# Kernel optimization log

Hardware: AMD Instinct MI355X
Metric: run time of the kernel (lower is better)

Reference implementation:

```python
import jax, jax.numpy as jnp
import numpy as np

N = 2048      # number of ROIs
C = 1024      # in_channels == inter_channels
G = 16        # groups
D = C // G    # per-group dim = 64


def _bbox_overlaps(b1, b2):
    # mmdet-1.x IoU with +1 pixel convention; b1:(N,4), b2:(M,4)
    area1 = (b1[:, 2] - b1[:, 0] + 1) * (b1[:, 3] - b1[:, 1] + 1)  # (N,)
    area2 = (b2[:, 2] - b2[:, 0] + 1) * (b2[:, 3] - b2[:, 1] + 1)  # (M,)
    lt = jnp.maximum(b1[:, None, :2], b2[None, :, :2])             # (N,M,2)
    rb = jnp.minimum(b1[:, None, 2:], b2[None, :, 2:])             # (N,M,2)
    wh = jnp.clip(rb - lt + 1, 0)
    inter = wh[..., 0] * wh[..., 1]                                # (N,M)
    return inter / (area1[:, None] + area2[None, :] - inter)


def setup_inputs() -> dict:
    key = jax.random.key(0)
    ks = jax.random.split(key, 9)
    in_x = jax.random.normal(ks[0], (N, C), dtype=jnp.float32)
    # valid boxes: [batch_idx, x1, y1, x2, y2]
    xy = jax.random.uniform(ks[1], (N, 2), minval=0.0, maxval=800.0)
    wh = jax.random.uniform(ks[2], (N, 2), minval=8.0, maxval=200.0)
    rois = jnp.concatenate([jnp.zeros((N, 1)), xy, xy + wh], axis=1).astype(jnp.float32)
    s = 1.0 / np.sqrt(C)
    W0 = jax.random.normal(ks[3], (C, C), dtype=jnp.float32) * s
    b0 = jnp.zeros((C,), dtype=jnp.float32)
    W1 = jax.random.normal(ks[4], (C, C), dtype=jnp.float32) * s
    b1 = jnp.zeros((C,), dtype=jnp.float32)
    # grouped 1x1 conv: per group maps C channels -> D channels
    Wout = jax.random.normal(ks[5], (G, D, C), dtype=jnp.float32) * s
    bout = jnp.zeros((C,), dtype=jnp.float32)
    return {"in_x": in_x, "rois": rois, "W0": W0, "b0": b0, "W1": W1,
            "b1": b1, "Wout": Wout, "bout": bout}


def reference(in_x, rois, W0, b0, W1, b1, Wout, bout):
    # self-attention path: in_ref_x = in_x, ref_rois = rois
    # embed convs are pre-activation (relu -> 1x1 conv), shared for x and ref_x
    def embed(v):
        v = jax.nn.relu(v) @ W0.T + b0
        v = jax.nn.relu(v) @ W1.T + b1
        return v
    x = embed(in_x)                      # (N, C)
    ref_x = x                            # shared convs, same input
    xg = x.reshape(N, G, D)
    rg = ref_x.reshape(N, G, D)
    scores = jnp.einsum('ngd,mgd->ngm', xg, rg) / jnp.sqrt(jnp.float32(D))  # (N,G,N)
    ious = _bbox_overlaps(rois[:, 1:], rois[:, 1:])                          # (N,N)
    scores = scores + jnp.log(ious[:, None, :] + 1e-6)
    attn = jax.nn.softmax(scores, axis=2)                                    # (N,G,N)
    y = jnp.einsum('ngm,mc->ngc', attn, in_x)                                # (N,G,C)
    out = jnp.einsum('ngc,goc->ngo', y, Wout).reshape(N, C) + bout           # (N,C)
    return out
```

## Files before the change

### kernel.cpp

```cpp
#include <hip/hip_runtime.h>
#include <math.h>

constexpr int NROI = 2048;
constexpr int CDIM = 1024;
constexpr int NG   = 16;
constexpr int DH   = 64;

typedef __attribute__((ext_vector_type(8))) short short8;
typedef __attribute__((ext_vector_type(4))) float floatx4;

#define MFMA_BF16(a, b, c) __builtin_amdgcn_mfma_f32_16x16x32_bf16((a), (b), (c), 0, 0, 0)

__device__ __forceinline__ short f2bf(float f) {
  unsigned u = __float_as_uint(f);
  unsigned r = 0x7fffu + ((u >> 16) & 1u);
  return (short)((u + r) >> 16);
}
__device__ __forceinline__ float bf2f(unsigned short u) {
  return __uint_as_float(((unsigned)u) << 16);
}
__device__ __forceinline__ unsigned pack2(float a, float b) {
  return (unsigned)(unsigned short)f2bf(a) | ((unsigned)(unsigned short)f2bf(b) << 16);
}

typedef __attribute__((address_space(1))) void GV;
typedef __attribute__((address_space(3))) void LV;
__device__ __forceinline__ void gl2lds16(const void* g, void* l) {
  __builtin_amdgcn_global_load_lds((GV*)g, (LV*)l, 16, 0, 0);
}

__device__ __forceinline__ short8 brelu(short8 v) {
  union { short8 s; unsigned u[4]; } x; x.s = v;
#pragma unroll
  for (int i = 0; i < 4; ++i) {
    unsigned m = (x.u[i] >> 15) & 0x10001u;
    x.u[i] &= ~(m * 0xFFFFu);
  }
  return x.s;
}

__global__ __launch_bounds__(256) void convert_kernel(
    const float* __restrict__ in_x, const float* __restrict__ W0,
    const float* __restrict__ W1, const float* __restrict__ Wout,
    short* __restrict__ xin_b, short* __restrict__ W0b,
    short* __restrict__ W1b, short* __restrict__ Woutb)
{
  const int i = blockIdx.x * 256 + threadIdx.x;
  {
    const float4 v = ((const float4*)in_x)[i];
    uint2 u; u.x = pack2(v.x, v.y); u.y = pack2(v.z, v.w);
    ((uint2*)xin_b)[i] = u;
  }
  if (i < 262144) {
    float4 v = ((const float4*)W0)[i];
    uint2 u; u.x = pack2(v.x, v.y); u.y = pack2(v.z, v.w);
    ((uint2*)W0b)[i] = u;
    v = ((const float4*)W1)[i];
    u.x = pack2(v.x, v.y); u.y = pack2(v.z, v.w);
    ((uint2*)W1b)[i] = u;
    v = ((const float4*)Wout)[i];
    u.x = pack2(v.x, v.y); u.y = pack2(v.z, v.w);
    ((uint2*)Woutb)[i] = u;
  }
}

__global__ __launch_bounds__(256) void iou_kernel(const float* __restrict__ rois,
                                                  unsigned short* __restrict__ biasb)
{
  const int q = blockIdx.y;
  const int k = blockIdx.x * 256 + threadIdx.x;
  const float qx1 = rois[q * 5 + 1], qy1 = rois[q * 5 + 2];
  const float qx2 = rois[q * 5 + 3], qy2 = rois[q * 5 + 4];
  const float qa = (qx2 - qx1 + 1.f) * (qy2 - qy1 + 1.f);
  const float kx1 = rois[k * 5 + 1], ky1 = rois[k * 5 + 2];
  const float kx2 = rois[k * 5 + 3], ky2 = rois[k * 5 + 4];
  const float ka = (kx2 - kx1 + 1.f) * (ky2 - ky1 + 1.f);
  float iw = fminf(qx2, kx2) - fmaxf(qx1, kx1) + 1.f;
  float ih = fminf(qy2, ky2) - fmaxf(qy1, ky1) + 1.f;
  iw = fmaxf(iw, 0.f); ih = fmaxf(ih, 0.f);
  const float inter = iw * ih;
  const float iou = inter / (qa + ka - inter);
  biasb[(size_t)q * NROI + k] = (unsigned short)f2bf(iou + 1e-6f);
}

__global__ __launch_bounds__(256) void gemm_bf16(
    const short* __restrict__ A, const short* __restrict__ B,
    const float* __restrict__ bias, short* __restrict__ C,
    int M, int Nn, int K, int reluA, int transOut)
{
  __shared__ short As[8 * 512];
  __shared__ short Bs[8 * 512];
  const int t = threadIdx.x, w = t >> 6, lane = t & 63;
  const int wm = w >> 1, wn = w & 1;
  const int row0 = blockIdx.y * 64, col0 = blockIdx.x * 64;
  const int rlo = lane & 15, khi = (lane >> 4) * 8;

  floatx4 acc[2][2];
#pragma unroll
  for (int i = 0; i < 2; ++i)
#pragma unroll
    for (int j = 0; j < 2; ++j) acc[i][j] = (floatx4){0.f, 0.f, 0.f, 0.f};

  for (int k0 = 0; k0 < K; k0 += 64) {
    __syncthreads();
#pragma unroll
    for (int kh = 0; kh < 2; ++kh) {
      gl2lds16(A + (size_t)(row0 + w * 16 + rlo) * K + k0 + kh * 32 + khi,
               &As[(w * 2 + kh) * 512]);
      gl2lds16(B + (size_t)(col0 + w * 16 + rlo) * K + k0 + kh * 32 + khi,
               &Bs[(w * 2 + kh) * 512]);
    }
    __syncthreads();
#pragma unroll
    for (int kh = 0; kh < 2; ++kh) {
      short8 a0 = *(const short8*)&As[((wm * 2 + 0) * 2 + kh) * 512 + lane * 8];
      short8 a1 = *(const short8*)&As[((wm * 2 + 1) * 2 + kh) * 512 + lane * 8];
      if (reluA) { a0 = brelu(a0); a1 = brelu(a1); }
      const short8 b0 = *(const short8*)&Bs[((wn * 2 + 0) * 2 + kh) * 512 + lane * 8];
      const short8 b1 = *(const short8*)&Bs[((wn * 2 + 1) * 2 + kh) * 512 + lane * 8];
      acc[0][0] = MFMA_BF16(a0, b0, acc[0][0]);
      acc[0][1] = MFMA_BF16(a0, b1, acc[0][1]);
      acc[1][0] = MFMA_BF16(a1, b0, acc[1][0]);
      acc[1][1] = MFMA_BF16(a1, b1, acc[1][1]);
    }
  }

  const int colL = lane & 15, qq = lane >> 4;
  float bj[2] = {0.f, 0.f};
  if (bias) {
    bj[0] = bias[col0 + wn * 32 + colL];
    bj[1] = bias[col0 + wn * 32 + 16 + colL];
  }
#pragma unroll
  for (int i = 0; i < 2; ++i)
#pragma unroll
    for (int j = 0; j < 2; ++j)
#pragma unroll
      for (int r = 0; r < 4; ++r) {
        const int row = row0 + wm * 32 + i * 16 + qq * 4 + r;
        const int cc  = col0 + wn * 32 + j * 16 + colL;
        const short bv = f2bf(acc[i][j][r] + bj[j]);
        if (transOut) C[(size_t)cc * M + row] = bv;
        else          C[(size_t)row * Nn + cc] = bv;
      }
}

__global__ __launch_bounds__(512) void attn_bias(
    const short* __restrict__ Xb,
    const short* __restrict__ ZTb,
    const unsigned short* __restrict__ biasb,
    const float* __restrict__ bout,
    float* __restrict__ Out)
{
  const int g  = blockIdx.y;
  const int n0 = blockIdx.x * 128;
  const int t  = threadIdx.x;
  const int w    = t >> 6;
  const int lane = t & 63;
  const int col  = lane & 15;
  const int qq   = lane >> 4;
  const int t16 = (w >> 1) * 16;
  const int h32 = (w & 1) * 32;
  const int rlo = lane & 15, khi = (lane >> 4) * 8;

  __shared__ short Kf[2][8 * 512];
  __shared__ short Vf[2][8 * 512];
  __shared__ short Pf[8 * 1024];

  const size_t qoff = (size_t)(n0 + w * 16 + col) * CDIM + g * DH;
  const short8 qf0 = *(const short8*)(Xb + qoff + qq * 8);
  const short8 qf1 = *(const short8*)(Xb + qoff + 32 + qq * 8);

  floatx4 oc[4];
#pragma unroll
  for (int dt = 0; dt < 4; ++dt) oc[dt] = (floatx4){0.f, 0.f, 0.f, 0.f};
  float lsum[4] = {0.f, 0.f, 0.f, 0.f};

  gl2lds16(Xb + (size_t)(t16 + rlo) * CDIM + g * DH + h32 + khi, &Kf[0][w * 512]);
  gl2lds16(ZTb + (size_t)(g * DH + t16 + rlo) * NROI + h32 + khi, &Vf[0][w * 512]);
  __syncthreads();

  for (int it = 0; it < NROI / 64; ++it) {
    const int p  = it & 1;
    const int m0 = it * 64;
    if (it + 1 < NROI / 64) {
      const int m1 = m0 + 64;
      gl2lds16(Xb + (size_t)(m1 + t16 + rlo) * CDIM + g * DH + h32 + khi,
               &Kf[1 - p][w * 512]);
      gl2lds16(ZTb + (size_t)(g * DH + t16 + rlo) * NROI + m1 + h32 + khi,
               &Vf[1 - p][w * 512]);
    }

    float bb[4][4];
#pragma unroll
    for (int ct = 0; ct < 4; ++ct)
#pragma unroll
      for (int r = 0; r < 4; ++r)
        bb[ct][r] = bf2f(biasb[(size_t)(n0 + w * 16 + qq * 4 + r) * NROI +
                               m0 + ct * 16 + col]);

    floatx4 sc[4];
#pragma unroll
    for (int ct = 0; ct < 4; ++ct) {
      const short8 b0 = *(const short8*)&Kf[p][(ct * 2 + 0) * 512 + lane * 8];
      const short8 b1 = *(const short8*)&Kf[p][(ct * 2 + 1) * 512 + lane * 8];
      floatx4 z4 = (floatx4){0.f, 0.f, 0.f, 0.f};
      z4 = MFMA_BF16(qf0, b0, z4);
      z4 = MFMA_BF16(qf1, b1, z4);
      sc[ct] = z4;
    }

#pragma unroll
    for (int ct = 0; ct < 4; ++ct)
#pragma unroll
      for (int r = 0; r < 4; ++r)
        sc[ct][r] = __expf(sc[ct][r] * 0.125f) * bb[ct][r];
#pragma unroll
    for (int r = 0; r < 4; ++r)
      lsum[r] += sc[0][r] + sc[1][r] + sc[2][r] + sc[3][r];

    {
      short* pw = &Pf[w * 1024];
#pragma unroll
      for (int ct = 0; ct < 4; ++ct) {
        const int key = ct * 16 + col;
        const int base = (key >> 5) * 512 + (key & 7);
#pragma unroll
        for (int r = 0; r < 4; ++r) {
          const int dl = (4 * qq + r) + ((key >> 3) & 3) * 16;
          pw[base + dl * 8] = f2bf(sc[ct][r]);
        }
      }
      const short8 pa0 = *(const short8*)&pw[0 * 512 + lane * 8];
      const short8 pa1 = *(const short8*)&pw[1 * 512 + lane * 8];
#pragma unroll
      for (int dt = 0; dt < 4; ++dt) {
        const short8 v0 = *(const short8*)&Vf[p][(dt * 2 + 0) * 512 + lane * 8];
        const short8 v1 = *(const short8*)&Vf[p][(dt * 2 + 1) * 512 + lane * 8];
        oc[dt] = MFMA_BF16(pa0, v0, oc[dt]);
        oc[dt] = MFMA_BF16(pa1, v1, oc[dt]);
      }
    }
    __syncthreads();
  }

#pragma unroll
  for (int r = 0; r < 4; ++r) {
    float s = lsum[r];
    s += __shfl_xor(s, 1); s += __shfl_xor(s, 2);
    s += __shfl_xor(s, 4); s += __shfl_xor(s, 8);
    lsum[r] = s;
  }
#pragma unroll
  for (int dt = 0; dt < 4; ++dt) {
    const float bo = bout[g * DH + dt * 16 + col];
#pragma unroll
    for (int r = 0; r < 4; ++r)
      Out[(size_t)(n0 + w * 16 + qq * 4 + r) * CDIM + g * DH + dt * 16 + col] =
          oc[dt][r] / lsum[r] + bo;
  }
}

__global__ __launch_bounds__(256) void attn_inline(
    const short* __restrict__ Xb, const short* __restrict__ ZTb,
    const float* __restrict__ rois, const float* __restrict__ bout,
    float* __restrict__ Out)
{
  const int g = blockIdx.y, n0 = blockIdx.x * 64;
  const int t = threadIdx.x, w = t >> 6, lane = t & 63;
  const int col = lane & 15, qq = lane >> 4;

  __shared__ short Kf[8 * 512];
  __shared__ short Vf[8 * 512];
  __shared__ short Pf[4 * 1024];
  __shared__ float Bsb[64 * 5];

  const size_t qoff = (size_t)(n0 + w * 16 + col) * CDIM + g * DH;
  const short8 qf0 = *(const short8*)(Xb + qoff + qq * 8);
  const short8 qf1 = *(const short8*)(Xb + qoff + 32 + qq * 8);

  float qx1[4], qy1[4], qx2[4], qy2[4], qar[4];
#pragma unroll
  for (int r = 0; r < 4; ++r) {
    const float* rb = rois + (size_t)(n0 + w * 16 + qq * 4 + r) * 5;
    qx1[r] = rb[1]; qy1[r] = rb[2]; qx2[r] = rb[3]; qy2[r] = rb[4];
    qar[r] = (qx2[r] - qx1[r] + 1.f) * (qy2[r] - qy1[r] + 1.f);
  }

  floatx4 oc[4];
#pragma unroll
  for (int dt = 0; dt < 4; ++dt) oc[dt] = (floatx4){0.f, 0.f, 0.f, 0.f};
  float lsum[4] = {0.f, 0.f, 0.f, 0.f};

  for (int m0 = 0; m0 < NROI; m0 += 64) {
    __syncthreads();
#pragma unroll
    for (int ss = 0; ss < 2; ++ss) {
      const int s = t + ss * 256;
      {
        const int key = s >> 3, d0 = (s & 7) * 8;
        const int fr = (key >> 4) * 2 + (d0 >> 5);
        const int dl = (key & 15) + ((d0 >> 3) & 3) * 16;
        *(short8*)&Kf[fr * 512 + dl * 8] =
            *(const short8*)(Xb + (size_t)(m0 + key) * CDIM + g * DH + d0);
      }
      {
        const int d = s >> 3, k0 = (s & 7) * 8;
        const int fr = (d >> 4) * 2 + (k0 >> 5);
        const int dl = (d & 15) + ((k0 >> 3) & 3) * 16;
        *(short8*)&Vf[fr * 512 + dl * 8] =
            *(const short8*)(ZTb + (size_t)(g * DH + d) * NROI + m0 + k0);
      }
    }
    if (t < 64) {
      const float* rb = rois + (size_t)(m0 + t) * 5;
      const float x1 = rb[1], y1 = rb[2], x2 = rb[3], y2 = rb[4];
      Bsb[t * 5 + 0] = x1; Bsb[t * 5 + 1] = y1;
      Bsb[t * 5 + 2] = x2; Bsb[t * 5 + 3] = y2;
      Bsb[t * 5 + 4] = (x2 - x1 + 1.f) * (y2 - y1 + 1.f);
    }
    __syncthreads();

    floatx4 sc[4];
#pragma unroll
    for (int ct = 0; ct < 4; ++ct) {
      const short8 b0 = *(const short8*)&Kf[(ct * 2 + 0) * 512 + lane * 8];
      const short8 b1 = *(const short8*)&Kf[(ct * 2 + 1) * 512 + lane * 8];
      floatx4 z4 = (floatx4){0.f, 0.f, 0.f, 0.f};
      z4 = MFMA_BF16(qf0, b0, z4);
      z4 = MFMA_BF16(qf1, b1, z4);
      sc[ct] = z4;
    }
#pragma unroll
    for (int ct = 0; ct < 4; ++ct) {
      const int k = ct * 16 + col;
      const float kx1 = Bsb[k * 5 + 0], ky1 = Bsb[k * 5 + 1];
      const float kx2 = Bsb[k * 5 + 2], ky2 = Bsb[k * 5 + 3], ka = Bsb[k * 5 + 4];
#pragma unroll
      for (int r = 0; r < 4; ++r) {
        float iw = fminf(qx2[r], kx2) - fmaxf(qx1[r], kx1) + 1.f;
        float ih = fminf(qy2[r], ky2) - fmaxf(qy1[r], ky1) + 1.f;
        iw = fmaxf(iw, 0.f); ih = fmaxf(ih, 0.f);
        const float inter = iw * ih;
        const float iou = inter * __builtin_amdgcn_rcpf(qar[r] + ka - inter);
        sc[ct][r] = __expf(sc[ct][r] * 0.125f) * (iou + 1e-6f);
      }
    }
#pragma unroll
    for (int r = 0; r < 4; ++r)
      lsum[r] += sc[0][r] + sc[1][r] + sc[2][r] + sc[3][r];
    {
      short* pw = &Pf[w * 1024];
#pragma unroll
      for (int ct = 0; ct < 4; ++ct) {
        const int key = ct * 16 + col;
        const int base = (key >> 5) * 512 + (key & 7);
#pragma unroll
        for (int r = 0; r < 4; ++r) {
          const int dl = (4 * qq + r) + ((key >> 3) & 3) * 16;
          pw[base + dl * 8] = f2bf(sc[ct][r]);
        }
      }
      const short8 pa0 = *(const short8*)&pw[0 * 512 + lane * 8];
      const short8 pa1 = *(const short8*)&pw[1 * 512 + lane * 8];
#pragma unroll
      for (int dt = 0; dt < 4; ++dt) {
        const short8 v0 = *(const short8*)&Vf[(dt * 2 + 0) * 512 + lane * 8];
        const short8 v1 = *(const short8*)&Vf[(dt * 2 + 1) * 512 + lane * 8];
        oc[dt] = MFMA_BF16(pa0, v0, oc[dt]);
        oc[dt] = MFMA_BF16(pa1, v1, oc[dt]);
      }
    }
  }

#pragma unroll
  for (int r = 0; r < 4; ++r) {
    float s = lsum[r];
    s += __shfl_xor(s, 1); s += __shfl_xor(s, 2);
    s += __shfl_xor(s, 4); s += __shfl_xor(s, 8);
    lsum[r] = s;
  }
#pragma unroll
  for (int dt = 0; dt < 4; ++dt) {
    const float bo = bout[g * DH + dt * 16 + col];
#pragma unroll
    for (int r = 0; r < 4; ++r)
      Out[(size_t)(n0 + w * 16 + qq * 4 + r) * CDIM + g * DH + dt * 16 + col] =
          oc[dt][r] / lsum[r] + bo;
  }
}

extern "C" void kernel_launch(void* const* d_in, const int* in_sizes, int n_in,
                              void* d_out, int out_size, void* d_ws, size_t ws_size,
                              hipStream_t stream) {
  const float* in_x = (const float*)d_in[0];
  const float* rois = (const float*)d_in[1];
  const float* W0   = (const float*)d_in[2];
  const float* b0   = (const float*)d_in[3];
  const float* W1   = (const float*)d_in[4];
  const float* b1   = (const float*)d_in[5];
  const float* Wout = (const float*)d_in[6];
  const float* bout = (const float*)d_in[7];
  float* out = (float*)d_out;
  char* w8 = (char*)d_ws;

  short* xin_b = (short*)(w8);
  short* W0b   = (short*)(w8 + (4u << 20));
  short* W1b   = (short*)(w8 + (6u << 20));
  short* Woutb = (short*)(w8 + (8u << 20));
  short* zT    = (short*)(w8 + (10u << 20));
  unsigned short* biasb = (unsigned short*)(w8 + (14u << 20));
  short* xb  = xin_b;
  short* t0b = (short*)d_out;
  const bool useBias = ws_size >= ((size_t)22u << 20);

  convert_kernel<<<2048, 256, 0, stream>>>(in_x, W0, W1, Wout,
                                           xin_b, W0b, W1b, Woutb);
  if (useBias)
    iou_kernel<<<dim3(NROI / 256, NROI), 256, 0, stream>>>(rois, biasb);

  const dim3 gg(CDIM / 64, NROI / 64);
  gemm_bf16<<<gg, 256, 0, stream>>>(xin_b, W0b, b0, t0b,
                                    NROI, CDIM, CDIM, 1, 0);
  gemm_bf16<<<gg, 256, 0, stream>>>(xin_b, Woutb, nullptr, zT,
                                    NROI, CDIM, CDIM, 0, 1);
  gemm_bf16<<<gg, 256, 0, stream>>>(t0b, W1b, b1, xb,
                                    NROI, CDIM, CDIM, 1, 0);

  if (useBias)
    attn_bias<<<dim3(NROI / 128, NG), 512, 0, stream>>>(xb, zT, biasb, bout, out);
  else
    attn_inline<<<dim3(NROI / 64, NG), 256, 0, stream>>>(xb, zT, rois, bout, out);
}
```

Baseline: 200.2 us.

## Split attention over key halves, fuse first GEMMs, transpose IoU bias loads

The attention kernel is split along the key dimension into two halves, doubling the number of blocks. Each half writes partial outputs (fp32 for one, bf16 for the other) and row sums, and a new merge kernel normalises them and adds the output bias. The IoU bias is read through the matrix's symmetry as contiguous uint2 vectors, prefetched one tile ahead. The two GEMMs that share the input are fused into one launch, and workspace buffers are reused in place. The costs are an extra merge pass, bf16 rounding of one partial sum, a larger fixed workspace requirement, and removal of the inline-IoU fallback path.

```diff
diff --git a/kernel.cpp b/kernel.cpp
--- a/kernel.cpp
+++ b/kernel.cpp
@@ -15,9 +15,6 @@
   unsigned u = __float_as_uint(f);
   unsigned r = 0x7fffu + ((u >> 16) & 1u);
   return (short)((u + r) >> 16);
-}
-__device__ __forceinline__ float bf2f(unsigned short u) {
-  return __uint_as_float(((unsigned)u) << 16);
 }
 __device__ __forceinline__ unsigned pack2(float a, float b) {
   return (unsigned)(unsigned short)f2bf(a) | ((unsigned)(unsigned short)f2bf(b) << 16);
@@ -83,10 +80,74 @@
   biasb[(size_t)q * NROI + k] = (unsigned short)f2bf(iou + 1e-6f);
 }
 
-__global__ __launch_bounds__(256) void gemm_bf16(
+__global__ __launch_bounds__(256) void gemm_fusedA(
+    const short* __restrict__ A, const short* __restrict__ BW0,
+    const short* __restrict__ BWout, const float* __restrict__ b0,
+    short* __restrict__ t0b, short* __restrict__ zT)
+{
+  __shared__ short As[8 * 512];
+  __shared__ short Bs[8 * 512];
+  const int isW0 = blockIdx.x < 16;
+  const int col0 = (blockIdx.x & 15) * 64;
+  const short* B = isW0 ? BW0 : BWout;
+  const int t = threadIdx.x, w = t >> 6, lane = t & 63;
+  const int wm = w >> 1, wn = w & 1;
+  const int row0 = blockIdx.y * 64;
+  const int rlo = lane & 15, khi = (lane >> 4) * 8;
+
+  floatx4 acc[2][2];
+#pragma unroll
+  for (int i = 0; i < 2; ++i)
+#pragma unroll
+    for (int j = 0; j < 2; ++j) acc[i][j] = (floatx4){0.f, 0.f, 0.f, 0.f};
+
+  for (int k0 = 0; k0 < CDIM; k0 += 64) {
+    __syncthreads();
+#pragma unroll
+    for (int kh = 0; kh < 2; ++kh) {
+      gl2lds16(A + (size_t)(row0 + w * 16 + rlo) * CDIM + k0 + kh * 32 + khi,
+               &As[(w * 2 + kh) * 512]);
+      gl2lds16(B + (size_t)(col0 + w * 16 + rlo) * CDIM + k0 + kh * 32 + khi,
+               &Bs[(w * 2 + kh) * 512]);
+    }
+    __syncthreads();
+#pragma unroll
+    for (int kh = 0; kh < 2; ++kh) {
+      short8 a0 = *(const short8*)&As[((wm * 2 + 0) * 2 + kh) * 512 + lane * 8];
+      short8 a1 = *(const short8*)&As[((wm * 2 + 1) * 2 + kh) * 512 + lane * 8];
+      if (isW0) { a0 = brelu(a0); a1 = brelu(a1); }
+      const short8 b0f = *(const short8*)&Bs[((wn * 2 + 0) * 2 + kh) * 512 + lane * 8];
+      const short8 b1f = *(const short8*)&Bs[((wn * 2 + 1) * 2 + kh) * 512 + lane * 8];
+      acc[0][0] = MFMA_BF16(a0, b0f, acc[0][0]);
+      acc[0][1] = MFMA_BF16(a0, b1f, acc[0][1]);
+      acc[1][0] = MFMA_BF16(a1, b0f, acc[1][0]);
+      acc[1][1] = MFMA_BF16(a1, b1f, acc[1][1]);
+    }
+  }
+
+  const int colL = lane & 15, qq = lane >> 4;
+  float bj[2] = {0.f, 0.f};
+  if (isW0) {
+    bj[0] = b0[col0 + wn * 32 + colL];
+    bj[1] = b0[col0 + wn * 32 + 16 + colL];
+  }
+#pragma unroll
+  for (int i = 0; i < 2; ++i)
+#pragma unroll
+    for (int j = 0; j < 2; ++j)
+#pragma unroll
+      for (int r = 0; r < 4; ++r) {
+        const int row = row0 + wm * 32 + i * 16 + qq * 4 + r;
+        const int cc  = col0 + wn * 32 + j * 16 + colL;
+        const short bv = f2bf(acc[i][j][r] + bj[j]);
+        if (isW0) t0b[(size_t)row * CDIM + cc] = bv;
+        else      zT[(size_t)cc * NROI + row] = bv;
+      }
+}
+
+__global__ __launch_bounds__(256) void gemm_relu_nt(
     const short* __restrict__ A, const short* __restrict__ B,
-    const float* __restrict__ bias, short* __restrict__ C,
-    int M, int Nn, int K, int reluA, int transOut)
+    const float* __restrict__ bias, short* __restrict__ C)
 {
   __shared__ short As[8 * 512];
   __shared__ short Bs[8 * 512];
@@ -101,13 +162,13 @@
 #pragma unroll
     for (int j = 0; j < 2; ++j) acc[i][j] = (floatx4){0.f, 0.f, 0.f, 0.f};
 
-  for (int k0 = 0; k0 < K; k0 += 64) {
+  for (int k0 = 0; k0 < CDIM; k0 += 64) {
     __syncthreads();
 #pragma unroll
     for (int kh = 0; kh < 2; ++kh) {
-      gl2lds16(A + (size_t)(row0 + w * 16 + rlo) * K + k0 + kh * 32 + khi,
+      gl2lds16(A + (size_t)(row0 + w * 16 + rlo) * CDIM + k0 + kh * 32 + khi,
                &As[(w * 2 + kh) * 512]);
-      gl2lds16(B + (size_t)(col0 + w * 16 + rlo) * K + k0 + kh * 32 + khi,
+      gl2lds16(B + (size_t)(col0 + w * 16 + rlo) * CDIM + k0 + kh * 32 + khi,
                &Bs[(w * 2 + kh) * 512]);
     }
     __syncthreads();
@@ -115,22 +176,20 @@
     for (int kh = 0; kh < 2; ++kh) {
       short8 a0 = *(const short8*)&As[((wm * 2 + 0) * 2 + kh) * 512 + lane * 8];
       short8 a1 = *(const short8*)&As[((wm * 2 + 1) * 2 + kh) * 512 + lane * 8];
-      if (reluA) { a0 = brelu(a0); a1 = brelu(a1); }
-      const short8 b0 = *(const short8*)&Bs[((wn * 2 + 0) * 2 + kh) * 512 + lane * 8];
-      const short8 b1 = *(const short8*)&Bs[((wn * 2 + 1) * 2 + kh) * 512 + lane * 8];
-      acc[0][0] = MFMA_BF16(a0, b0, acc[0][0]);
-      acc[0][1] = MFMA_BF16(a0, b1, acc[0][1]);
-      acc[1][0] = MFMA_BF16(a1, b0, acc[1][0]);
-      acc[1][1] = MFMA_BF16(a1, b1, acc[1][1]);
+      a0 = brelu(a0); a1 = brelu(a1);
+      const short8 b0f = *(const short8*)&Bs[((wn * 2 + 0) * 2 + kh) * 512 + lane * 8];
+      const short8 b1f = *(const short8*)&Bs[((wn * 2 + 1) * 2 + kh) * 512 + lane * 8];
+      acc[0][0] = MFMA_BF16(a0, b0f, acc[0][0]);
+      acc[0][1] = MFMA_BF16(a0, b1f, acc[0][1]);
+      acc[1][0] = MFMA_BF16(a1, b0f, acc[1][0]);
+      acc[1][1] = MFMA_BF16(a1, b1f, acc[1][1]);
     }
   }
 
   const int colL = lane & 15, qq = lane >> 4;
-  float bj[2] = {0.f, 0.f};
-  if (bias) {
-    bj[0] = bias[col0 + wn * 32 + colL];
-    bj[1] = bias[col0 + wn * 32 + 16 + colL];
-  }
+  float bj[2];
+  bj[0] = bias[col0 + wn * 32 + colL];
+  bj[1] = bias[col0 + wn * 32 + 16 + colL];
 #pragma unroll
   for (int i = 0; i < 2; ++i)
 #pragma unroll
@@ -139,28 +198,24 @@
       for (int r = 0; r < 4; ++r) {
         const int row = row0 + wm * 32 + i * 16 + qq * 4 + r;
         const int cc  = col0 + wn * 32 + j * 16 + colL;
-        const short bv = f2bf(acc[i][j][r] + bj[j]);
-        if (transOut) C[(size_t)cc * M + row] = bv;
-        else          C[(size_t)row * Nn + cc] = bv;
+        C[(size_t)row * CDIM + cc] = f2bf(acc[i][j][r] + bj[j]);
       }
 }
 
-__global__ __launch_bounds__(512) void attn_bias(
+__global__ __launch_bounds__(512) void attn_split(
     const short* __restrict__ Xb,
     const short* __restrict__ ZTb,
     const unsigned short* __restrict__ biasb,
-    const float* __restrict__ bout,
-    float* __restrict__ Out)
+    float* __restrict__ O0, short* __restrict__ O1,
+    float* __restrict__ lsums)
 {
   const int g  = blockIdx.y;
   const int n0 = blockIdx.x * 128;
-  const int t  = threadIdx.x;
-  const int w    = t >> 6;
-  const int lane = t & 63;
-  const int col  = lane & 15;
-  const int qq   = lane >> 4;
-  const int t16 = (w >> 1) * 16;
-  const int h32 = (w & 1) * 32;
+  const int sp = blockIdx.z;
+  const int mbase = sp * 1024;
+  const int t = threadIdx.x, w = t >> 6, lane = t & 63;
+  const int col = lane & 15, qq = lane >> 4;
+  const int t16 = (w >> 1) * 16, h32 = (w & 1) * 32;
   const int rlo = lane & 15, khi = (lane >> 4) * 8;
 
   __shared__ short Kf[2][8 * 512];
@@ -176,28 +231,29 @@
   for (int dt = 0; dt < 4; ++dt) oc[dt] = (floatx4){0.f, 0.f, 0.f, 0.f};
   float lsum[4] = {0.f, 0.f, 0.f, 0.f};
 
-  gl2lds16(Xb + (size_t)(t16 + rlo) * CDIM + g * DH + h32 + khi, &Kf[0][w * 512]);
-  gl2lds16(ZTb + (size_t)(g * DH + t16 + rlo) * NROI + h32 + khi, &Vf[0][w * 512]);
+  const int qrow0 = n0 + w * 16 + qq * 4;
+
+  uint2 bbc[4], bbn[4];
+#pragma unroll
+  for (int ct = 0; ct < 4; ++ct)
+    bbc[ct] = *(const uint2*)(biasb + (size_t)(mbase + ct * 16 + col) * NROI + qrow0);
+
+  gl2lds16(Xb + (size_t)(mbase + t16 + rlo) * CDIM + g * DH + h32 + khi, &Kf[0][w * 512]);
+  gl2lds16(ZTb + (size_t)(g * DH + t16 + rlo) * NROI + mbase + h32 + khi, &Vf[0][w * 512]);
   __syncthreads();
 
-  for (int it = 0; it < NROI / 64; ++it) {
-    const int p  = it & 1;
-    const int m0 = it * 64;
-    if (it + 1 < NROI / 64) {
-      const int m1 = m0 + 64;
+  for (int it = 0; it < 16; ++it) {
+    const int p = it & 1;
+    if (it < 15) {
+      const int m1 = mbase + (it + 1) * 64;
       gl2lds16(Xb + (size_t)(m1 + t16 + rlo) * CDIM + g * DH + h32 + khi,
                &Kf[1 - p][w * 512]);
       gl2lds16(ZTb + (size_t)(g * DH + t16 + rlo) * NROI + m1 + h32 + khi,
                &Vf[1 - p][w * 512]);
-    }
-
-    float bb[4][4];
-#pragma unroll
-    for (int ct = 0; ct < 4; ++ct)
-#pragma unroll
-      for (int r = 0; r < 4; ++r)
-        bb[ct][r] = bf2f(biasb[(size_t)(n0 + w * 16 + qq * 4 + r) * NROI +
-                               m0 + ct * 16 + col]);
+#pragma unroll
+      for (int ct = 0; ct < 4; ++ct)
+        bbn[ct] = *(const uint2*)(biasb + (size_t)(m1 + ct * 16 + col) * NROI + qrow0);
+    }
 
     floatx4 sc[4];
 #pragma unroll
@@ -211,10 +267,13 @@
     }
 
 #pragma unroll
-    for (int ct = 0; ct < 4; ++ct)
-#pragma unroll
-      for (int r = 0; r < 4; ++r)
-        sc[ct][r] = __expf(sc[ct][r] * 0.125f) * bb[ct][r];
+    for (int ct = 0; ct < 4; ++ct) {
+      const unsigned ux = bbc[ct].x, uy = bbc[ct].y;
+      sc[ct][0] = __expf(sc[ct][0] * 0.125f) * __uint_as_float(ux << 16);
+      sc[ct][1] = __expf(sc[ct][1] * 0.125f) * __uint_as_float(ux & 0xFFFF0000u);
+      sc[ct][2] = __expf(sc[ct][2] * 0.125f) * __uint_as_float(uy << 16);
+      sc[ct][3] = __expf(sc[ct][3] * 0.125f) * __uint_as_float(uy & 0xFFFF0000u);
+    }
 #pragma unroll
     for (int r = 0; r < 4; ++r)
       lsum[r] += sc[0][r] + sc[1][r] + sc[2][r] + sc[3][r];
@@ -242,6 +301,8 @@
       }
     }
     __syncthreads();
+#pragma unroll
+    for (int ct = 0; ct < 4; ++ct) bbc[ct] = bbn[ct];
   }
 
 #pragma unroll
@@ -251,143 +312,44 @@
     s += __shfl_xor(s, 4); s += __shfl_xor(s, 8);
     lsum[r] = s;
   }
-#pragma unroll
-  for (int dt = 0; dt < 4; ++dt) {
-    const float bo = bout[g * DH + dt * 16 + col];
+  if (col == 0) {
 #pragma unroll
     for (int r = 0; r < 4; ++r)
-      Out[(size_t)(n0 + w * 16 + qq * 4 + r) * CDIM + g * DH + dt * 16 + col] =
-          oc[dt][r] / lsum[r] + bo;
-  }
-}
-
-__global__ __launch_bounds__(256) void attn_inline(
-    const short* __restrict__ Xb, const short* __restrict__ ZTb,
-    const float* __restrict__ rois, const float* __restrict__ bout,
+      lsums[sp * (NG * NROI) + g * NROI + qrow0 + r] = lsum[r];
+  }
+  if (sp == 0) {
+#pragma unroll
+    for (int dt = 0; dt < 4; ++dt)
+#pragma unroll
+      for (int r = 0; r < 4; ++r)
+        O0[(size_t)(qrow0 + r) * CDIM + g * DH + dt * 16 + col] = oc[dt][r];
+  } else {
+#pragma unroll
+    for (int dt = 0; dt < 4; ++dt)
+#pragma unroll
+      for (int r = 0; r < 4; ++r)
+        O1[(size_t)(qrow0 + r) * CDIM + g * DH + dt * 16 + col] = f2bf(oc[dt][r]);
+  }
+}
+
+__global__ __launch_bounds__(256) void merge_kernel(
+    const float* __restrict__ O0, const short* __restrict__ O1,
+    const float* __restrict__ lsums, const float* __restrict__ bout,
     float* __restrict__ Out)
 {
-  const int g = blockIdx.y, n0 = blockIdx.x * 64;
-  const int t = threadIdx.x, w = t >> 6, lane = t & 63;
-  const int col = lane & 15, qq = lane >> 4;
-
-  __shared__ short Kf[8 * 512];
-  __shared__ short Vf[8 * 512];
-  __shared__ short Pf[4 * 1024];
-  __shared__ float Bsb[64 * 5];
-
-  const size_t qoff = (size_t)(n0 + w * 16 + col) * CDIM + g * DH;
-  const short8 qf0 = *(const short8*)(Xb + qoff + qq * 8);
-  const short8 qf1 = *(const short8*)(Xb + qoff + 32 + qq * 8);
-
-  float qx1[4], qy1[4], qx2[4], qy2[4], qar[4];
-#pragma unroll
-  for (int r = 0; r < 4; ++r) {
-    const float* rb = rois + (size_t)(n0 + w * 16 + qq * 4 + r) * 5;
-    qx1[r] = rb[1]; qy1[r] = rb[2]; qx2[r] = rb[3]; qy2[r] = rb[4];
-    qar[r] = (qx2[r] - qx1[r] + 1.f) * (qy2[r] - qy1[r] + 1.f);
-  }
-
-  floatx4 oc[4];
-#pragma unroll
-  for (int dt = 0; dt < 4; ++dt) oc[dt] = (floatx4){0.f, 0.f, 0.f, 0.f};
-  float lsum[4] = {0.f, 0.f, 0.f, 0.f};
-
-  for (int m0 = 0; m0 < NROI; m0 += 64) {
-    __syncthreads();
-#pragma unroll
-    for (int ss = 0; ss < 2; ++ss) {
-      const int s = t + ss * 256;
-      {
-        const int key = s >> 3, d0 = (s & 7) * 8;
-        const int fr = (key >> 4) * 2 + (d0 >> 5);
-        const int dl = (key & 15) + ((d0 >> 3) & 3) * 16;
-        *(short8*)&Kf[fr * 512 + dl * 8] =
-            *(const short8*)(Xb + (size_t)(m0 + key) * CDIM + g * DH + d0);
-      }
-      {
-        const int d = s >> 3, k0 = (s & 7) * 8;
-        const int fr = (d >> 4) * 2 + (k0 >> 5);
-        const int dl = (d & 15) + ((k0 >> 3) & 3) * 16;
-        *(short8*)&Vf[fr * 512 + dl * 8] =
-            *(const short8*)(ZTb + (size_t)(g * DH + d) * NROI + m0 + k0);
-      }
-    }
-    if (t < 64) {
-      const float* rb = rois + (size_t)(m0 + t) * 5;
-      const float x1 = rb[1], y1 = rb[2], x2 = rb[3], y2 = rb[4];
-      Bsb[t * 5 + 0] = x1; Bsb[t * 5 + 1] = y1;
-      Bsb[t * 5 + 2] = x2; Bsb[t * 5 + 3] = y2;
-      Bsb[t * 5 + 4] = (x2 - x1 + 1.f) * (y2 - y1 + 1.f);
-    }
-    __syncthreads();
-
-    floatx4 sc[4];
-#pragma unroll
-    for (int ct = 0; ct < 4; ++ct) {
-      const short8 b0 = *(const short8*)&Kf[(ct * 2 + 0) * 512 + lane * 8];
-      const short8 b1 = *(const short8*)&Kf[(ct * 2 + 1) * 512 + lane * 8];
-      floatx4 z4 = (floatx4){0.f, 0.f, 0.f, 0.f};
-      z4 = MFMA_BF16(qf0, b0, z4);
-      z4 = MFMA_BF16(qf1, b1, z4);
-      sc[ct] = z4;
-    }
-#pragma unroll
-    for (int ct = 0; ct < 4; ++ct) {
-      const int k = ct * 16 + col;
-      const float kx1 = Bsb[k * 5 + 0], ky1 = Bsb[k * 5 + 1];
-      const float kx2 = Bsb[k * 5 + 2], ky2 = Bsb[k * 5 + 3], ka = Bsb[k * 5 + 4];
-#pragma unroll
-      for (int r = 0; r < 4; ++r) {
-        float iw = fminf(qx2[r], kx2) - fmaxf(qx1[r], kx1) + 1.f;
-        float ih = fminf(qy2[r], ky2) - fmaxf(qy1[r], ky1) + 1.f;
-        iw = fmaxf(iw, 0.f); ih = fmaxf(ih, 0.f);
-        const float inter = iw * ih;
-        const float iou = inter * __builtin_amdgcn_rcpf(qar[r] + ka - inter);
-        sc[ct][r] = __expf(sc[ct][r] * 0.125f) * (iou + 1e-6f);
-      }
-    }
-#pragma unroll
-    for (int r = 0; r < 4; ++r)
-      lsum[r] += sc[0][r] + sc[1][r] + sc[2][r] + sc[3][r];
-    {
-      short* pw = &Pf[w * 1024];
-#pragma unroll
-      for (int ct = 0; ct < 4; ++ct) {
-        const int key = ct * 16 + col;
-        const int base = (key >> 5) * 512 + (key & 7);
-#pragma unroll
-        for (int r = 0; r < 4; ++r) {
-          const int dl = (4 * qq + r) + ((key >> 3) & 3) * 16;
-          pw[base + dl * 8] = f2bf(sc[ct][r]);
-        }
-      }
-      const short8 pa0 = *(const short8*)&pw[0 * 512 + lane * 8];
-      const short8 pa1 = *(const short8*)&pw[1 * 512 + lane * 8];
-#pragma unroll
-      for (int dt = 0; dt < 4; ++dt) {
-        const short8 v0 = *(const short8*)&Vf[(dt * 2 + 0) * 512 + lane * 8];
-        const short8 v1 = *(const short8*)&Vf[(dt * 2 + 1) * 512 + lane * 8];
-        oc[dt] = MFMA_BF16(pa0, v0, oc[dt]);
-        oc[dt] = MFMA_BF16(pa1, v1, oc[dt]);
-      }
-    }
-  }
-
-#pragma unroll
-  for (int r = 0; r < 4; ++r) {
-    float s = lsum[r];
-    s += __shfl_xor(s, 1); s += __shfl_xor(s, 2);
-    s += __shfl_xor(s, 4); s += __shfl_xor(s, 8);
-    lsum[r] = s;
-  }
-#pragma unroll
-  for (int dt = 0; dt < 4; ++dt) {
-    const float bo = bout[g * DH + dt * 16 + col];
-#pragma unroll
-    for (int r = 0; r < 4; ++r)
-      Out[(size_t)(n0 + w * 16 + qq * 4 + r) * CDIM + g * DH + dt * 16 + col] =
-          oc[dt][r] / lsum[r] + bo;
-  }
+  const int i = blockIdx.x * 256 + threadIdx.x;
+  const int base = i * 4, q = base >> 10, c = base & 1023, g = c >> 6;
+  const float l = lsums[g * NROI + q] + lsums[NG * NROI + g * NROI + q];
+  const float linv = 1.f / l;
+  const float4 o0 = ((const float4*)O0)[i];
+  const uint2 o1 = ((const uint2*)O1)[i];
+  const float4 bo = *(const float4*)(bout + c);
+  float4 o;
+  o.x = (o0.x + __uint_as_float(o1.x << 16))          * linv + bo.x;
+  o.y = (o0.y + __uint_as_float(o1.x & 0xFFFF0000u))  * linv + bo.y;
+  o.z = (o0.z + __uint_as_float(o1.y << 16))          * linv + bo.z;
+  o.w = (o0.w + __uint_as_float(o1.y & 0xFFFF0000u))  * linv + bo.w;
+  ((float4*)Out)[i] = o;
 }
 
 extern "C" void kernel_launch(void* const* d_in, const int* in_sizes, int n_in,
@@ -401,34 +363,25 @@
   const float* b1   = (const float*)d_in[5];
   const float* Wout = (const float*)d_in[6];
   const float* bout = (const float*)d_in[7];
-  float* out = (float*)d_out;
   char* w8 = (char*)d_ws;
 
-  short* xin_b = (short*)(w8);
+  short* xin_b = (short*)w8;
   short* W0b   = (short*)(w8 + (4u << 20));
-  short* W1b   = (short*)(w8 + (6u << 20));
-  short* Woutb = (short*)(w8 + (8u << 20));
-  short* zT    = (short*)(w8 + (10u << 20));
-  unsigned short* biasb = (unsigned short*)(w8 + (14u << 20));
+  short* Woutb = (short*)(w8 + (6u << 20));
+  unsigned short* biasb = (unsigned short*)(w8 + (4u << 20));
+  short* zT    = (short*)(w8 + (12u << 20));
+  short* O1    = (short*)(w8 + (16u << 20));
+  short* W1b   = (short*)(w8 + (20u << 20));
+  float* lsums = (float*)(w8 + (20u << 20));
   short* xb  = xin_b;
   short* t0b = (short*)d_out;
-  const bool useBias = ws_size >= ((size_t)22u << 20);
+  float* O0  = (float*)d_out;
 
   convert_kernel<<<2048, 256, 0, stream>>>(in_x, W0, W1, Wout,
                                            xin_b, W0b, W1b, Woutb);
-  if (useBias)
-    iou_kernel<<<dim3(NROI / 256, NROI), 256, 0, stream>>>(rois, biasb);
-
-  const dim3 gg(CDIM / 64, NROI / 64);
-  gemm_bf16<<<gg, 256, 0, stream>>>(xin_b, W0b, b0, t0b,
-                                    NROI, CDIM, CDIM, 1, 0);
-  gemm_bf16<<<gg, 256, 0, stream>>>(xin_b, Woutb, nullptr, zT,
-                                    NROI, CDIM, CDIM, 0, 1);
-  gemm_bf16<<<gg, 256, 0, stream>>>(t0b, W1b, b1, xb,
-                                    NROI, CDIM, CDIM, 1, 0);
-
-  if (useBias)
-    attn_bias<<<dim3(NROI / 128, NG), 512, 0, stream>>>(xb, zT, biasb, bout, out);
-  else
-    attn_inline<<<dim3(NROI / 64, NG), 256, 0, stream>>>(xb, zT, rois, bout, out);
-}
+  gemm_fusedA<<<dim3(32, 32), 256, 0, stream>>>(xin_b, W0b, Woutb, b0, t0b, zT);
+  iou_kernel<<<dim3(NROI / 256, NROI), 256, 0, stream>>>(rois, biasb);
+  gemm_relu_nt<<<dim3(16, 32), 256, 0, stream>>>(t0b, W1b, b1, xb);
+  attn_split<<<dim3(NROI / 128, NG, 2), 512, 0, stream>>>(xb, zT, biasb, O0, O1, lsums);
+  merge_kernel<<<2048, 256, 0, stream>>>(O0, O1, lsums, bout, (float*)d_out);
+}
```

Result: no change. 201.1 us (+0.4%).
